# Kernel tuning notes

Measured on AMD Instinct MI355X. Metric: run time of the kernel, lower is better.

Reference implementation:

```python
import jax, jax.numpy as jnp
import numpy as np

D = 1024
H = 16
HD = D // H
FF = 4096
B, S = 2, 2048


def _ln(x, g, b, eps):
    mu = jnp.mean(x, axis=-1, keepdims=True)
    var = jnp.mean(jnp.square(x - mu), axis=-1, keepdims=True)
    return (x - mu) * jax.lax.rsqrt(var + eps) * g + b


def setup_inputs() -> dict:
    key = jax.random.key(0)
    ks = jax.random.split(key, 12)
    s = 0.02
    return {
        "x": jax.random.normal(ks[0], (B, S, D), jnp.float32),
        "attention_mask": jnp.ones((B, 1, 1, S), jnp.int32),
        "wq": jax.random.normal(ks[1], (D, D), jnp.float32) * s,
        "bq": jnp.zeros((D,), jnp.float32),
        "wk": jax.random.normal(ks[2], (D, D), jnp.float32) * s,
        "bk": jnp.zeros((D,), jnp.float32),
        "wv": jax.random.normal(ks[3], (D, D), jnp.float32) * s,
        "bv": jnp.zeros((D,), jnp.float32),
        "wo": jax.random.normal(ks[4], (D, D), jnp.float32) * s,
        "bo": jnp.zeros((D,), jnp.float32),
        "ln1_g": jnp.ones((D,), jnp.float32),
        "ln1_b": jnp.zeros((D,), jnp.float32),
        "w1": jax.random.normal(ks[5], (D, FF), jnp.float32) * s,
        "b1": jnp.zeros((FF,), jnp.float32),
        "w2": jax.random.normal(ks[6], (FF, D), jnp.float32) * s,
        "b2": jnp.zeros((D,), jnp.float32),
        "lnf_g": jnp.ones((D,), jnp.float32),
        "lnf_b": jnp.zeros((D,), jnp.float32),
        "ln2_g": jnp.ones((D,), jnp.float32),
        "ln2_b": jnp.zeros((D,), jnp.float32),
    }


def reference(x, attention_mask, wq, bq, wk, bk, wv, bv, wo, bo,
              ln1_g, ln1_b, w1, b1, w2, b2, lnf_g, lnf_b, ln2_g, ln2_b):
    b, s, d = x.shape
    # --- naive multi-head self-attention ---
    q = (x @ wq + bq).reshape(b, s, H, HD).transpose(0, 2, 1, 3)  # [b,h,s,hd]
    k = (x @ wk + bk).reshape(b, s, H, HD).transpose(0, 2, 1, 3)
    v = (x @ wv + bv).reshape(b, s, H, HD).transpose(0, 2, 1, 3)
    scores = jnp.einsum('bhqd,bhkd->bhqk', q, k) / jnp.sqrt(jnp.float32(HD))
    scores = jnp.where(attention_mask == 0, jnp.float32(-1e9), scores)
    attn = jax.nn.softmax(scores, axis=-1)
    ctx = jnp.einsum('bhqk,bhkd->bhqd', attn, v)
    ctx = ctx.transpose(0, 2, 1, 3).reshape(b, s, d)
    attn_out = ctx @ wo + bo
    # residual + LayerNorm (eps=1e-5, torch default)
    x1 = _ln(x + attn_out, ln1_g, ln1_b, 1e-5)
    # --- BERT-style FFN with internal residual LN (eps=1e-12) ---
    h = jax.nn.gelu(x1 @ w1 + b1, approximate=False)
    ff = _ln(h @ w2 + b2 + x1, lnf_g, lnf_b, 1e-12)
    # --- outer residual + LayerNorm (eps=1e-5) ---
    return _ln(x1 + ff, ln2_g, ln2_b, 1e-5)
```

## Files before the change

kernel.cpp:

```cpp
#include <hip/hip_runtime.h>

#define DMODEL 1024
#define NHEAD  16
#define HDIM   64
#define FFDIM  4096
#define BATCH  2
#define SEQ    2048
#define MTOK   (BATCH*SEQ)

typedef __bf16 bf16;
typedef __bf16 bf16x8 __attribute__((ext_vector_type(8)));
typedef __bf16 bf16x4 __attribute__((ext_vector_type(4)));
typedef float  floatx4 __attribute__((ext_vector_type(4)));
typedef unsigned int u32;
typedef unsigned int u32x4 __attribute__((ext_vector_type(4)));

__device__ __forceinline__ int get_flag(const void* ln1g) {
  return (((const u32*)ln1g)[0] == 0x3F800000u) ? 0 : 1;
}
__device__ __forceinline__ float ld_ext(const void* p, size_t i, int flag) {
  return flag ? (float)((const bf16*)p)[i] : ((const float*)p)[i];
}

__device__ __forceinline__ void gload16(const bf16* g, bf16* lds_uniform) {
  __builtin_amdgcn_global_load_lds(
      (const __attribute__((address_space(1))) u32*)g,
      (__attribute__((address_space(3))) u32*)lds_uniform, 16, 0, 0);
}

__device__ __forceinline__ float gelu_f(float v) {
  float e = __expf(-1.702f * v);
  return __fdividef(v, 1.0f + e);
}

#define VMW(n) asm volatile("s_waitcnt vmcnt(" #n ")" ::: "memory")

__global__ __launch_bounds__(256) void prep(
    const void* wq, const void* wk, const void* wv, const void* wo,
    const void* w1, const void* w2, const void* x, const int* mask,
    bf16* WTqkv, bf16* WToT, bf16* WT1, bf16* WT2, bf16* xC,
    u32* mwAll, bf16* m01All, const void* ln1g)
{
  int flag = get_flag(ln1g);
  int bid = blockIdx.x;
  if (bid >= 16384) {
    int b = bid - 16384;
    int base = b * SEQ + threadIdx.x * 8;
    #pragma unroll
    for (int j = 0; j < 8; j++)
      m01All[base + j] = (bf16)(mask[base + j] ? 1.0f : 0.0f);
    #pragma unroll
    for (int t = 0; t < 4; t++) {
      int k0 = threadIdx.x * 8 + 2 * t;
      u32 mw = (mask[b * SEQ + k0] ? 0x0000FFFFu : 0u) |
               (mask[b * SEQ + k0 + 1] ? 0xFFFF0000u : 0u);
      mwAll[b * (SEQ / 2) + threadIdx.x * 4 + t] = mw;
    }
    return;
  }
  if (bid >= 12288) {
    size_t base = (size_t)(bid - 12288) * 1024;
    int i = threadIdx.x * 4;
    #pragma unroll
    for (int j = 0; j < 4; j++) xC[base + i + j] = (bf16)ld_ext(x, base + i + j, flag);
    return;
  }
  __shared__ bf16 tile[32][33];
  const void* in; bf16* out; int K, N, t;
  if      (bid < 1024)  { in = wq; out = WTqkv;                 K = 1024; N = 1024; t = bid; }
  else if (bid < 2048)  { in = wk; out = WTqkv + 1024 * 1024;   K = 1024; N = 1024; t = bid - 1024; }
  else if (bid < 3072)  { in = wv; out = WTqkv + 2 * 1024 * 1024; K = 1024; N = 1024; t = bid - 2048; }
  else if (bid < 4096)  { in = wo; out = WToT;                  K = 1024; N = 1024; t = bid - 3072; }
  else if (bid < 8192)  { in = w1; out = WT1;                   K = 1024; N = 4096; t = bid - 4096; }
  else                  { in = w2; out = WT2;                   K = 4096; N = 1024; t = bid - 8192; }
  int shift = (N == 4096) ? 7 : 5;
  int k0 = (t >> shift) * 32, n0 = (t & ((1 << shift) - 1)) * 32;
  int tx = threadIdx.x & 31, ty = threadIdx.x >> 5;
  #pragma unroll
  for (int i = ty; i < 32; i += 8)
    tile[i][tx] = (bf16)ld_ext(in, (size_t)(k0 + i) * N + n0 + tx, flag);
  __syncthreads();
  #pragma unroll
  for (int i = ty; i < 32; i += 8)
    out[(size_t)(n0 + i) * K + k0 + tx] = tile[tx][i];
}

__global__ __launch_bounds__(256) void gemm128(
    const bf16* __restrict__ A, const bf16* __restrict__ BT,
    const void* __restrict__ bias0, const void* __restrict__ bias1,
    const void* __restrict__ bias2,
    bf16* __restrict__ out0, bf16* __restrict__ out1, bf16* __restrict__ out2,
    int N, int K, int ksub, int mode, const void* __restrict__ ln1g)
{
  __shared__ __align__(16) char smem[32768];
  bf16* As = (bf16*)smem;
  bf16* Bs = (bf16*)(smem + 16384);
  int flag = get_flag(ln1g);

  int tid = threadIdx.x, lane = tid & 63, w = tid >> 6;
  int wm = w & 1, wn = w >> 1;
  int m0 = blockIdx.x * 128, n0 = blockIdx.y * 128;
  int kstart = blockIdx.z * ksub;
  int r15 = lane & 15, kg = lane >> 4;

  floatx4 acc[4][4];
  #pragma unroll
  for (int mt = 0; mt < 4; mt++)
    #pragma unroll
    for (int nt = 0; nt < 4; nt++) acc[mt][nt] = (floatx4){0.f, 0.f, 0.f, 0.f};

  int srow8 = lane >> 3;
  int skc = (lane & 7) ^ (srow8 & 7);
  const bf16* Ap = A  + (size_t)(m0 + w * 32 + srow8) * K + kstart + skc * 8;
  const bf16* Bp = BT + (size_t)(n0 + w * 32 + srow8) * K + kstart + skc * 8;
  const size_t jstr = (size_t)8 * K;

  for (int it = ksub >> 6; it > 0; it--) {
    #pragma unroll
    for (int j = 0; j < 4; j++) {
      gload16(Ap + j * jstr, As + (size_t)(w * 256 + j * 64) * 8);
      gload16(Bp + j * jstr, Bs + (size_t)(w * 256 + j * 64) * 8);
    }
    Ap += 64; Bp += 64;
    __syncthreads();

    #pragma unroll
    for (int kk = 0; kk < 2; kk++) {
      bf16x8 af[4], bfr[4];
      #pragma unroll
      for (int mt = 0; mt < 4; mt++) {
        int row = wm * 64 + mt * 16 + r15;
        int slot = (kk * 4 + kg) ^ (r15 & 7);
        af[mt] = *(const bf16x8*)&As[(row * 8 + slot) * 8];
      }
      #pragma unroll
      for (int nt = 0; nt < 4; nt++) {
        int row = wn * 64 + nt * 16 + r15;
        int slot = (kk * 4 + kg) ^ (r15 & 7);
        bfr[nt] = *(const bf16x8*)&Bs[(row * 8 + slot) * 8];
      }
      #pragma unroll
      for (int mt = 0; mt < 4; mt++)
        #pragma unroll
        for (int nt = 0; nt < 4; nt++)
          acc[mt][nt] = __builtin_amdgcn_mfma_f32_16x16x32_bf16(af[mt], bfr[nt], acc[mt][nt], 0, 0, 0);
    }
    __syncthreads();
  }

  bf16* scr = (bf16*)(smem + 5120 * w);
  int gcb = n0 + wn * 64;
  int which = (mode == 1) ? (gcb >> 10) : 0;
  int rowg0 = m0 + wm * 64;
  bf16* outp = out0 + (size_t)blockIdx.z * MTOK * N;

  float bvs[4];
  #pragma unroll
  for (int nt = 0; nt < 4; nt++) {
    int gcol = gcb + nt * 16 + r15;
    int bidx = (mode == 1) ? (gcol & 1023) : gcol;
    const void* bp = (mode == 1) ? ((which == 0) ? bias0 : (which == 1) ? bias1 : bias2) : bias0;
    bvs[nt] = (blockIdx.z == 0) ? ld_ext(bp, bidx, flag) : 0.f;
  }

  #pragma unroll
  for (int pass = 0; pass < 2; pass++) {
    #pragma unroll
    for (int mh = 0; mh < 2; mh++) {
      int mt = 2 * pass + mh;
      #pragma unroll
      for (int nt = 0; nt < 4; nt++) {
        int lcol = nt * 16 + r15;
        #pragma unroll
        for (int r = 0; r < 4; r++) {
          int lrow = mh * 16 + kg * 4 + r;
          float val = acc[mt][nt][r] + bvs[nt];
          if (mode == 2) val = gelu_f(val);
          if (mode == 1 && which == 0) val *= 0.125f;
          if (mode == 1 && which == 2) scr[lcol * 40 + lrow] = (bf16)val;
          else                         scr[lrow * 68 + lcol] = (bf16)val;
        }
      }
    }
    if (mode == 1 && which == 2) {
      int hh = (gcb - 2048) >> 6;
      int b = rowg0 >> 11, s0 = rowg0 & 2047;
      #pragma unroll
      for (int it = 0; it < 4; it++) {
        int c = it * 64 + lane;
        int cc = c >> 2, part = c & 3;
        bf16x8 vdat = *(const bf16x8*)&scr[cc * 40 + part * 8];
        *(bf16x8*)(out2 + ((size_t)(b * NHEAD + hh) * HDIM + cc) * SEQ + s0 + pass * 32 + part * 8) = vdat;
      }
    } else {
      #pragma unroll
      for (int it = 0; it < 4; it++) {
        int c = it * 64 + lane;
        int rr = c >> 3, part = c & 7;
        bf16x8 vdat = *(const bf16x8*)&scr[rr * 68 + part * 8];
        int rowg = rowg0 + pass * 32 + rr;
        bf16* dst;
        if (mode == 1) {
          int b = rowg >> 11, s = rowg & 2047;
          int hh = (gcb & 1023) >> 6;
          bf16* o = (which == 0) ? out0 : out1;
          dst = o + ((size_t)(b * NHEAD + hh) * SEQ + s) * HDIM + part * 8;
        } else {
          dst = outp + (size_t)rowg * N + gcb + part * 8;
        }
        *(bf16x8*)dst = vdat;
      }
    }
  }
}

#define STAGE_A(dstbuf, koff, qm)                                             \
  { int gch = (lane & 7) ^ (srow8 & 7);                                       \
    _Pragma("unroll") for (int j = 0; j < 2; j++) {                           \
      int rb = (qm) * 64 + j * 128 + w * 8;                                   \
      gload16(A + (size_t)(m0 + rb + srow8) * K + (koff) + gch * 8,           \
              (dstbuf) + (size_t)rb * 64);                                    \
    } }

#define STAGE_B(dstbuf, koff, qn)                                             \
  { int gch = (lane & 7) ^ (srow8 & 7);                                       \
    _Pragma("unroll") for (int j = 0; j < 2; j++) {                           \
      int rb = (2 * j + (w >> 2)) * 64 + (qn) * 32 + (w & 3) * 8;             \
      gload16(BT + (size_t)(n0 + rb + srow8) * K + (koff) + gch * 8,          \
              (dstbuf) + (size_t)rb * 64);                                    \
    } }

#define PHASE(QM, QN, STAGE_STMT, WAIT_STMT)                                  \
  {                                                                           \
    bf16x8 af[4][2], bfr[2][2];                                               \
    _Pragma("unroll") for (int mt = 0; mt < 4; mt++) {                        \
      int row = wm * 128 + (QM) * 64 + mt * 16 + r15;                         \
      _Pragma("unroll") for (int kk = 0; kk < 2; kk++) {                      \
        int slot = (kk * 4 + kg) ^ (r15 & 7);                                 \
        af[mt][kk] = *(const bf16x8*)&Ac[(size_t)(row * 8 + slot) * 8];       \
      }                                                                       \
    }                                                                         \
    _Pragma("unroll") for (int nt = 0; nt < 2; nt++) {                        \
      int row = wn * 64 + (QN) * 32 + nt * 16 + r15;                          \
      _Pragma("unroll") for (int kk = 0; kk < 2; kk++) {                      \
        int slot = (kk * 4 + kg) ^ (r15 & 7);                                 \
        bfr[nt][kk] = *(const bf16x8*)&Bc[(size_t)(row * 8 + slot) * 8];      \
      }                                                                       \
    }                                                                         \
    STAGE_STMT;                                                               \
    WAIT_STMT;                                                                \
    __builtin_amdgcn_s_barrier();                                             \
    asm volatile("" ::: "memory");                                            \
    __builtin_amdgcn_s_setprio(1);                                            \
    _Pragma("unroll") for (int kk = 0; kk < 2; kk++)                          \
      _Pragma("unroll") for (int mt = 0; mt < 4; mt++)                        \
        _Pragma("unroll") for (int nt = 0; nt < 2; nt++)                      \
          acc[(QM) * 4 + mt][(QN) * 2 + nt] =                                 \
              __builtin_amdgcn_mfma_f32_16x16x32_bf16(                        \
                  af[mt][kk], bfr[nt][kk],                                    \
                  acc[(QM) * 4 + mt][(QN) * 2 + nt], 0, 0, 0);                \
    __builtin_amdgcn_s_setprio(0);                                            \
    __builtin_amdgcn_s_barrier();                                             \
    asm volatile("" ::: "memory");                                            \
  }

__global__ __launch_bounds__(512, 2) void gemm256(
    const bf16* __restrict__ A, const bf16* __restrict__ BT,
    const void* __restrict__ bias0, const void* __restrict__ bias1,
    const void* __restrict__ bias2,
    bf16* __restrict__ out0, bf16* __restrict__ out1, bf16* __restrict__ out2,
    int N, int K, int ksub, int mode, const void* __restrict__ ln1g)
{
  __shared__ __align__(16) char smem[131072];
  int flag = get_flag(ln1g);

  int tid = threadIdx.x, lane = tid & 63, w = tid >> 6;
  int wm = w >> 2, wn = w & 3;
  int r15 = lane & 15, kg = lane >> 4;
  int srow8 = lane >> 3;

  int nx = gridDim.x, ny = gridDim.y;
  int nwg = nx * ny * gridDim.z;
  int wg = blockIdx.x + nx * (blockIdx.y + ny * blockIdx.z);
  if ((nwg & 7) == 0) wg = (wg & 7) * (nwg >> 3) + (wg >> 3);
  int bx = wg % nx, rem = wg / nx;
  int by = rem % ny, bz = rem / ny;

  int m0 = bx * 256, n0 = by * 256;
  int kstart = bz * ksub;
  int NT = ksub >> 6;

  floatx4 acc[8][4];
  #pragma unroll
  for (int mt = 0; mt < 8; mt++)
    #pragma unroll
    for (int nt = 0; nt < 4; nt++) acc[mt][nt] = (floatx4){0.f, 0.f, 0.f, 0.f};

  STAGE_A((bf16*)smem,             kstart, 0);
  STAGE_B((bf16*)(smem + 65536),   kstart, 0);
  STAGE_A((bf16*)smem,             kstart, 1);
  STAGE_B((bf16*)(smem + 65536),   kstart, 1);
  STAGE_A((bf16*)(smem + 32768),   kstart + 64, 0);
  STAGE_B((bf16*)(smem + 98304),   kstart + 64, 0);
  asm volatile("s_waitcnt vmcnt(4)" ::: "memory");
  __builtin_amdgcn_s_barrier();
  asm volatile("" ::: "memory");

  for (int t = 0; t < NT; t++) {
    int cur = (t & 1) * 32768, nxt = ((t + 1) & 1) * 32768;
    bf16* Ac = (bf16*)(smem + cur);
    bf16* Bc = (bf16*)(smem + 65536 + cur);
    bf16* An = (bf16*)(smem + nxt);
    bf16* Bn = (bf16*)(smem + 65536 + nxt);
    int t1 = (t + 1 < NT) ? t + 1 : NT - 1;
    int t2 = (t + 2 < NT) ? t + 2 : NT - 1;
    int k1 = kstart + t1 * 64, k2 = kstart + t2 * 64;
    PHASE(0, 0, STAGE_A(An, k1, 1), VMW(6));
    PHASE(0, 1, STAGE_B(Bn, k1, 1), );
    PHASE(1, 0, STAGE_A(Ac, k2, 0), );
    PHASE(1, 1, STAGE_B(Bc, k2, 0), VMW(8));
  }

  asm volatile("s_waitcnt vmcnt(0)" ::: "memory");
  __builtin_amdgcn_s_barrier();
  asm volatile("" ::: "memory");

  bf16* scr = (bf16*)(smem + 5120 * w);
  int gcb = n0 + wn * 64;
  int which = (mode == 1) ? (gcb >> 10) : 0;
  int rowg0 = m0 + wm * 128;
  bf16* outp = out0 + (size_t)bz * MTOK * (size_t)N;

  float bvs[4];
  #pragma unroll
  for (int nt = 0; nt < 4; nt++) {
    int gcol = gcb + nt * 16 + r15;
    int bidx = (mode == 1) ? (gcol & 1023) : gcol;
    const void* bp = (mode == 1) ? ((which == 0) ? bias0 : (which == 1) ? bias1 : bias2) : bias0;
    bvs[nt] = (bz == 0) ? ld_ext(bp, bidx, flag) : 0.f;
  }

  #pragma unroll
  for (int pass = 0; pass < 4; pass++) {
    #pragma unroll
    for (int mh = 0; mh < 2; mh++) {
      int mt = 2 * pass + mh;
      #pragma unroll
      for (int nt = 0; nt < 4; nt++) {
        int lcol = nt * 16 + r15;
        #pragma unroll
        for (int r = 0; r < 4; r++) {
          int lrow = mh * 16 + kg * 4 + r;
          float val = acc[mt][nt][r] + bvs[nt];
          if (mode == 2) val = gelu_f(val);
          if (mode == 1 && which == 0) val *= 0.125f;
          if (mode == 1 && which == 2) scr[lcol * 40 + lrow] = (bf16)val;
          else                         scr[lrow * 68 + lcol] = (bf16)val;
        }
      }
    }
    if (mode == 1 && which == 2) {
      int hh = (gcb - 2048) >> 6;
      int bb = rowg0 >> 11, s0 = rowg0 & 2047;
      #pragma unroll
      for (int it = 0; it < 4; it++) {
        int c = it * 64 + lane;
        int cc = c >> 2, part = c & 3;
        bf16x8 vdat = *(const bf16x8*)&scr[cc * 40 + part * 8];
        *(bf16x8*)(out2 + ((size_t)(bb * NHEAD + hh) * HDIM + cc) * SEQ + s0 + pass * 32 + part * 8) = vdat;
      }
    } else {
      #pragma unroll
      for (int it = 0; it < 4; it++) {
        int c = it * 64 + lane;
        int rr = c >> 3, part = c & 7;
        bf16x8 vdat = *(const bf16x8*)&scr[rr * 68 + part * 8];
        int rowg = rowg0 + pass * 32 + rr;
        bf16* dst;
        if (mode == 1) {
          int bb = rowg >> 11, s = rowg & 2047;
          int hh = (gcb & 1023) >> 6;
          bf16* o = (which == 0) ? out0 : out1;
          dst = o + ((size_t)(bb * NHEAD + hh) * SEQ + s) * HDIM + part * 8;
        } else {
          dst = outp + (size_t)rowg * N + gcb + part * 8;
        }
        *(bf16x8*)dst = vdat;
      }
    }
  }
}

__global__ __launch_bounds__(256) void attn_mfma(
    const bf16* __restrict__ q, const bf16* __restrict__ k,
    const bf16* __restrict__ vt, const u32* __restrict__ mwAll,
    const bf16* __restrict__ m01All, bf16* __restrict__ ctx)
{
  __shared__ __align__(16) bf16 Ks[2][4096];
  __shared__ __align__(16) bf16 Vts[2][4096];
  __shared__ __align__(16) bf16 Ps[4][2048];

  int tid = threadIdx.x, lane = tid & 63, w = tid >> 6;
  int r15 = lane & 15, kg = lane >> 4;
  int x7 = r15 & 7;
  int bh = (blockIdx.x & 7) * 4 + ((blockIdx.x >> 3) >> 4);
  int qt = (blockIdx.x >> 3) & 15;
  int b = bh >> 4, h = bh & 15;
  int q0 = qt * 128 + w * 32;

  bf16x8 qf[2][2];
  #pragma unroll
  for (int mt = 0; mt < 2; mt++)
    #pragma unroll
    for (int kt2 = 0; kt2 < 2; kt2++)
      qf[mt][kt2] = *(const bf16x8*)(q + ((size_t)bh * SEQ + q0 + mt * 16 + r15) * HDIM + kt2 * 32 + kg * 8);

  floatx4 O[2][4];
  floatx4 lacc[2];
  #pragma unroll
  for (int mt = 0; mt < 2; mt++) {
    lacc[mt] = (floatx4){0.f, 0.f, 0.f, 0.f};
    #pragma unroll
    for (int dt = 0; dt < 4; dt++) O[mt][dt] = (floatx4){0.f, 0.f, 0.f, 0.f};
  }

  int slo = kg ^ x7, shi = (kg + 4) ^ x7;
  const bf16* pap[2][2];
  #pragma unroll
  for (int mt = 0; mt < 2; mt++) {
    pap[mt][0] = &Ps[w][((mt * 16 + r15) * 8 + slo) * 8];
    pap[mt][1] = &Ps[w][((mt * 16 + r15) * 8 + shi) * 8];
  }

  int kr = lane >> 3, kc = lane & 7;
  int vrow = tid >> 3, vcc = tid & 7;
  int vsw = vcc ^ (vrow & 7);
  const bf16* kb_ = k + (size_t)bh * SEQ * HDIM;
  const bf16* vb_ = vt + (size_t)bh * HDIM * SEQ;
  const u32*  mwb = mwAll + (size_t)b * (SEQ / 2);
  const bf16* m1b = m01All + (size_t)b * SEQ;

  u32x4 pv0 = *(const u32x4*)(vb_ + (size_t)vrow * SEQ + vcc * 8);
  u32x4 pv1 = *(const u32x4*)(vb_ + (size_t)(vrow + 32) * SEQ + vcc * 8);
  u32x4 pmw = *(const u32x4*)&mwb[vcc * 4];
  bf16x8 m0c = *(const bf16x8*)&m1b[kg * 8];
  bf16x8 m1c = *(const bf16x8*)&m1b[32 + kg * 8];
  asm volatile("" ::: "memory");
  #pragma unroll
  for (int j = 0; j < 2; j++)
    gload16(kb_ + (size_t)(16 * w + 8 * j + kr) * HDIM + (kc ^ kr) * 8,
            &Ks[0][0] + (size_t)(w * 128 + j * 64) * 8);
  VMW(4);
  pv0 &= pmw; pv1 &= pmw;
  *(u32x4*)&Vts[0][(vrow * 8 + vsw) * 8] = pv0;
  *(u32x4*)&Vts[0][((vrow + 32) * 8 + vsw) * 8] = pv1;
  asm volatile("s_waitcnt lgkmcnt(0)" ::: "memory");
  __builtin_amdgcn_s_barrier();
  asm volatile("" ::: "memory");

  for (int t = 0; t < SEQ / 64; t++) {
    int cur = t & 1, nxt = cur ^ 1;
    int ktn = (t + 1 < SEQ / 64) ? (t + 1) * 64 : t * 64;
    u32x4 nv0 = *(const u32x4*)(vb_ + (size_t)vrow * SEQ + ktn + vcc * 8);
    u32x4 nv1 = *(const u32x4*)(vb_ + (size_t)(vrow + 32) * SEQ + ktn + vcc * 8);
    u32x4 nmw = *(const u32x4*)&mwb[(ktn + vcc * 8) >> 1];
    bf16x8 nm0 = *(const bf16x8*)&m1b[ktn + kg * 8];
    bf16x8 nm1 = *(const bf16x8*)&m1b[ktn + 32 + kg * 8];
    asm volatile("" ::: "memory");
    #pragma unroll
    for (int j = 0; j < 2; j++)
      gload16(kb_ + (size_t)(ktn + 16 * w + 8 * j + kr) * HDIM + (kc ^ kr) * 8,
              &Ks[nxt][0] + (size_t)(w * 128 + j * 64) * 8);
    VMW(7);
    __builtin_amdgcn_s_barrier();
    asm volatile("" ::: "memory");

    const bf16* Kc = &Ks[cur][0];
    const bf16* Vc = &Vts[cur][0];

    floatx4 S[2][4];
    #pragma unroll
    for (int mt = 0; mt < 2; mt++)
      #pragma unroll
      for (int nt = 0; nt < 4; nt++) S[mt][nt] = (floatx4){0.f, 0.f, 0.f, 0.f};
    __builtin_amdgcn_s_setprio(1);
    #pragma unroll
    for (int nt = 0; nt < 4; nt++) {
      int rb = (nt * 16 + r15) * 8;
      bf16x8 kf0 = *(const bf16x8*)&Kc[(rb + slo) * 8];
      bf16x8 kf1 = *(const bf16x8*)&Kc[(rb + shi) * 8];
      #pragma unroll
      for (int mt = 0; mt < 2; mt++) {
        S[mt][nt] = __builtin_amdgcn_mfma_f32_16x16x32_bf16(kf0, qf[mt][0], S[mt][nt], 0, 0, 0);
        S[mt][nt] = __builtin_amdgcn_mfma_f32_16x16x32_bf16(kf1, qf[mt][1], S[mt][nt], 0, 0, 0);
      }
    }
    __builtin_amdgcn_s_setprio(0);

    #pragma unroll
    for (int mt = 0; mt < 2; mt++)
      #pragma unroll
      for (int nt = 0; nt < 4; nt++) {
        bf16x4 pk;
        #pragma unroll
        for (int r = 0; r < 4; r++) pk[r] = (bf16)__expf(S[mt][nt][r]);
        int c2 = 2 * nt + (kg >> 1);
        *(bf16x4*)&Ps[w][((mt * 16 + r15) * 8 + (c2 ^ x7)) * 8 + (kg & 1) * 4] = pk;
      }

    bf16x8 pa[2][2];
    #pragma unroll
    for (int mt = 0; mt < 2; mt++) {
      pa[mt][0] = *(const bf16x8*)pap[mt][0];
      pa[mt][1] = *(const bf16x8*)pap[mt][1];
    }
    __builtin_amdgcn_s_setprio(1);
    #pragma unroll
    for (int dt = 0; dt < 4; dt++) {
      int rb = (dt * 16 + r15) * 8;
      bf16x8 vf0 = *(const bf16x8*)&Vc[(rb + slo) * 8];
      bf16x8 vf1 = *(const bf16x8*)&Vc[(rb + shi) * 8];
      #pragma unroll
      for (int mt = 0; mt < 2; mt++) {
        O[mt][dt] = __builtin_amdgcn_mfma_f32_16x16x32_bf16(pa[mt][0], vf0, O[mt][dt], 0, 0, 0);
        O[mt][dt] = __builtin_amdgcn_mfma_f32_16x16x32_bf16(pa[mt][1], vf1, O[mt][dt], 0, 0, 0);
      }
    }
    #pragma unroll
    for (int mt = 0; mt < 2; mt++) {
      lacc[mt] = __builtin_amdgcn_mfma_f32_16x16x32_bf16(pa[mt][0], m0c, lacc[mt], 0, 0, 0);
      lacc[mt] = __builtin_amdgcn_mfma_f32_16x16x32_bf16(pa[mt][1], m1c, lacc[mt], 0, 0, 0);
    }
    __builtin_amdgcn_s_setprio(0);

    VMW(2);
    nv0 &= nmw; nv1 &= nmw;
    *(u32x4*)&Vts[nxt][(vrow * 8 + vsw) * 8] = nv0;
    *(u32x4*)&Vts[nxt][((vrow + 32) * 8 + vsw) * 8] = nv1;
    m0c = nm0; m1c = nm1;
    asm volatile("s_waitcnt lgkmcnt(0)" ::: "memory");
    __builtin_amdgcn_s_barrier();
    asm volatile("" ::: "memory");
  }
  VMW(0);

  #pragma unroll
  for (int mt = 0; mt < 2; mt++) {
    float inv[4];
    #pragma unroll
    for (int r = 0; r < 4; r++) inv[r] = 1.f / lacc[mt][r];
    #pragma unroll
    for (int dt = 0; dt < 4; dt++)
      #pragma unroll
      for (int r = 0; r < 4; r++) {
        int srow = q0 + mt * 16 + kg * 4 + r;
        int col = h * 64 + dt * 16 + r15;
        ctx[((size_t)b * SEQ + srow) * DMODEL + col] = (bf16)(O[mt][dt][r] * inv[r]);
      }
  }
}

__global__ __launch_bounds__(256) void ln_kernel(
    const bf16* ba, const bf16* bb, const bf16* bc,
    const void* g, const void* be, float eps, bf16* outb, const void* ln1g)
{
  __shared__ float red1[4], red2[4];
  int flag = get_flag(ln1g);
  size_t base = (size_t)blockIdx.x * DMODEL;
  float v[4];
  #pragma unroll
  for (int i = 0; i < 4; i++) {
    int idx = threadIdx.x + i * 256;
    v[i] = (float)ba[base + idx] + (float)bb[base + idx] + (float)bc[base + idx];
  }
  float sum = v[0] + v[1] + v[2] + v[3];
  #pragma unroll
  for (int o = 32; o > 0; o >>= 1) sum += __shfl_xor(sum, o);
  if ((threadIdx.x & 63) == 0) red1[threadIdx.x >> 6] = sum;
  __syncthreads();
  float mean = (red1[0] + red1[1] + red1[2] + red1[3]) * (1.f / DMODEL);
  float sq = 0.f;
  #pragma unroll
  for (int i = 0; i < 4; i++) { v[i] -= mean; sq += v[i] * v[i]; }
  #pragma unroll
  for (int o = 32; o > 0; o >>= 1) sq += __shfl_xor(sq, o);
  if ((threadIdx.x & 63) == 0) red2[threadIdx.x >> 6] = sq;
  __syncthreads();
  float rstd = rsqrtf((red2[0] + red2[1] + red2[2] + red2[3]) * (1.f / DMODEL) + eps);
  #pragma unroll
  for (int i = 0; i < 4; i++) {
    int idx = threadIdx.x + i * 256;
    outb[base + idx] = (bf16)(v[i] * rstd * ld_ext(g, idx, flag) + ld_ext(be, idx, flag));
  }
}

__global__ __launch_bounds__(256) void ln_double(
    const bf16* p0, const bf16* p1, const bf16* p2, const bf16* p3,
    const bf16* x1,
    const void* gf, const void* bf, const void* g2, const void* b2,
    void* out_ext, const void* ln1g, int np)
{
  __shared__ float red1[4], red2[4];
  int flag = get_flag(ln1g);
  size_t base = (size_t)blockIdx.x * DMODEL;
  float xv[4], v[4];
  #pragma unroll
  for (int i = 0; i < 4; i++) {
    int idx = threadIdx.x + i * 256;
    xv[i] = (float)x1[base + idx];
    v[i] = xv[i] + (float)p0[base + idx] + (float)p1[base + idx];
    if (np == 4) v[i] += (float)p2[base + idx] + (float)p3[base + idx];
  }
  float sum = v[0] + v[1] + v[2] + v[3];
  #pragma unroll
  for (int o = 32; o > 0; o >>= 1) sum += __shfl_xor(sum, o);
  if ((threadIdx.x & 63) == 0) red1[threadIdx.x >> 6] = sum;
  __syncthreads();
  float mean = (red1[0] + red1[1] + red1[2] + red1[3]) * (1.f / DMODEL);
  float sq = 0.f;
  #pragma unroll
  for (int i = 0; i < 4; i++) { v[i] -= mean; sq += v[i] * v[i]; }
  #pragma unroll
  for (int o = 32; o > 0; o >>= 1) sq += __shfl_xor(sq, o);
  if ((threadIdx.x & 63) == 0) red2[threadIdx.x >> 6] = sq;
  __syncthreads();
  float rstd = rsqrtf((red2[0] + red2[1] + red2[2] + red2[3]) * (1.f / DMODEL) + 1e-12f);
  #pragma unroll
  for (int i = 0; i < 4; i++) {
    int idx = threadIdx.x + i * 256;
    float ff = v[i] * rstd * ld_ext(gf, idx, flag) + ld_ext(bf, idx, flag);
    v[i] = xv[i] + (float)(bf16)ff;
  }
  __syncthreads();
  sum = v[0] + v[1] + v[2] + v[3];
  #pragma unroll
  for (int o = 32; o > 0; o >>= 1) sum += __shfl_xor(sum, o);
  if ((threadIdx.x & 63) == 0) red1[threadIdx.x >> 6] = sum;
  __syncthreads();
  mean = (red1[0] + red1[1] + red1[2] + red1[3]) * (1.f / DMODEL);
  sq = 0.f;
  #pragma unroll
  for (int i = 0; i < 4; i++) { v[i] -= mean; sq += v[i] * v[i]; }
  #pragma unroll
  for (int o = 32; o > 0; o >>= 1) sq += __shfl_xor(sq, o);
  if ((threadIdx.x & 63) == 0) red2[threadIdx.x >> 6] = sq;
  __syncthreads();
  rstd = rsqrtf((red2[0] + red2[1] + red2[2] + red2[3]) * (1.f / DMODEL) + 1e-5f);
  #pragma unroll
  for (int i = 0; i < 4; i++) {
    int idx = threadIdx.x + i * 256;
    float y = v[i] * rstd * ld_ext(g2, idx, flag) + ld_ext(b2, idx, flag);
    if (flag) ((bf16*)out_ext)[base + idx] = (bf16)y;
    else      ((float*)out_ext)[base + idx] = y;
  }
}

extern "C" void kernel_launch(void* const* d_in, const int* in_sizes, int n_in,
                              void* d_out, int out_size, void* d_ws, size_t ws_size,
                              hipStream_t stream) {
  const void* x    = d_in[0];
  const int*  msk  = (const int*)d_in[1];
  const void* wq   = d_in[2];
  const void* bq   = d_in[3];
  const void* wk   = d_in[4];
  const void* bk   = d_in[5];
  const void* wv   = d_in[6];
  const void* bv   = d_in[7];
  const void* wo   = d_in[8];
  const void* bo   = d_in[9];
  const void* ln1g = d_in[10];
  const void* ln1b = d_in[11];
  const void* w1   = d_in[12];
  const void* b1   = d_in[13];
  const void* w2   = d_in[14];
  const void* b2   = d_in[15];
  const void* lnfg = d_in[16];
  const void* lnfb = d_in[17];
  const void* ln2g = d_in[18];
  const void* ln2b = d_in[19];

  const size_t MB = 1024 * 1024;
  char* p = (char*)d_ws;
  int big = ws_size >= (size_t)80 * MB;
  bf16* xC     = (bf16*)(p + 0 * MB);
  bf16* qb     = (bf16*)(p + 8 * MB);
  bf16* kb     = (bf16*)(p + 16 * MB);
  bf16* vtb    = (bf16*)(p + 24 * MB);
  bf16* ctxb   = (bf16*)(p + 32 * MB);
  bf16* WTqkv  = (bf16*)(p + 40 * MB);
  bf16* WToT   = (bf16*)(p + 46 * MB);
  bf16* WT1    = (bf16*)(p + 48 * MB);
  bf16* WT2    = (bf16*)(p + (big ? 72 : 56) * MB);
  bf16* ao     = (bf16*)(p + 8 * MB);
  bf16* x1b    = xC;
  bf16* hb     = (bf16*)(p + 8 * MB);
  bf16* ffp    = (bf16*)(p + 40 * MB);
  u32*  mwAll  = (u32*)d_out;
  bf16* m01All = (bf16*)((char*)d_out + 8192);
  const size_t PS = (size_t)MTOK * DMODEL;

  prep<<<16386, 256, 0, stream>>>(wq, wk, wv, wo, w1, w2, x, msk,
                                  WTqkv, WToT, WT1, WT2, xC, mwAll, m01All, ln1g);

  gemm256<<<dim3(MTOK / 256, 3072 / 256, 1), 512, 0, stream>>>(
      xC, WTqkv, bq, bk, bv, qb, kb, vtb, 3072, DMODEL, DMODEL, 1, ln1g);

  attn_mfma<<<BATCH * NHEAD * (SEQ / 128), 256, 0, stream>>>(qb, kb, vtb, mwAll, m01All, ctxb);

  gemm128<<<dim3(MTOK / 128, DMODEL / 128, 2), 256, 0, stream>>>(
      ctxb, WToT, bo, nullptr, nullptr, ao, nullptr, nullptr, DMODEL, DMODEL, 512, 3, ln1g);

  ln_kernel<<<MTOK, 256, 0, stream>>>(ao, ao + PS, xC, ln1g, ln1b,
                                      1e-5f, x1b, ln1g);

  gemm256<<<dim3(MTOK / 256, FFDIM / 256, 1), 512, 0, stream>>>(
      x1b, WT1, b1, nullptr, nullptr, hb, nullptr, nullptr, FFDIM, DMODEL, DMODEL, 2, ln1g);

  if (big) {
    gemm256<<<dim3(MTOK / 256, DMODEL / 256, 4), 512, 0, stream>>>(
        hb, WT2, b2, nullptr, nullptr, ffp, nullptr, nullptr, DMODEL, FFDIM, FFDIM / 4, 3, ln1g);
    ln_double<<<MTOK, 256, 0, stream>>>(ffp, ffp + PS, ffp + 2 * PS, ffp + 3 * PS,
                                        x1b, lnfg, lnfb, ln2g, ln2b, d_out, ln1g, 4);
  } else {
    gemm128<<<dim3(MTOK / 128, DMODEL / 128, 2), 256, 0, stream>>>(
        hb, WT2, b2, nullptr, nullptr, ffp, nullptr, nullptr, DMODEL, FFDIM, 2048, 3, ln1g);
    ln_double<<<MTOK, 256, 0, stream>>>(ffp, ffp + PS, ffp, ffp,
                                        x1b, lnfg, lnfb, ln2g, ln2b, d_out, ln1g, 2);
  }
}
```

Baseline: 376.9 us.

## Software-pipeline attention PV matmul one tile behind and route QKV GEMM to gemm128

The attention kernel now double-buffers the per-wave P tile and runs the P·V and row-sum MFMAs for the previous key tile alongside the QK^T MFMAs for the current one. This lets exp/softmax work overlap with matrix work, and it needs an epilogue step after the loop for the last tile. The QKV projection launch moves from gemm256 to gemm128, and gemm256 loses its mode-1 (QKV scatter) epilogue, which shrinks its argument list and branches. The pipelining adds LDS use and changes where the barrier sits, so it relies on the zero-initialised second buffers to make the first iteration's extra MFMAs harmless.

```diff
diff --git a/kernel.cpp b/kernel.cpp
--- a/kernel.cpp
+++ b/kernel.cpp
@@ -266,9 +266,7 @@
 
 __global__ __launch_bounds__(512, 2) void gemm256(
     const bf16* __restrict__ A, const bf16* __restrict__ BT,
-    const void* __restrict__ bias0, const void* __restrict__ bias1,
-    const void* __restrict__ bias2,
-    bf16* __restrict__ out0, bf16* __restrict__ out1, bf16* __restrict__ out2,
+    const void* __restrict__ bias0, bf16* __restrict__ out0,
     int N, int K, int ksub, int mode, const void* __restrict__ ln1g)
 {
   __shared__ __align__(16) char smem[131072];
@@ -327,7 +325,6 @@
 
   bf16* scr = (bf16*)(smem + 5120 * w);
   int gcb = n0 + wn * 64;
-  int which = (mode == 1) ? (gcb >> 10) : 0;
   int rowg0 = m0 + wm * 128;
   bf16* outp = out0 + (size_t)bz * MTOK * (size_t)N;
 
@@ -335,9 +332,7 @@
   #pragma unroll
   for (int nt = 0; nt < 4; nt++) {
     int gcol = gcb + nt * 16 + r15;
-    int bidx = (mode == 1) ? (gcol & 1023) : gcol;
-    const void* bp = (mode == 1) ? ((which == 0) ? bias0 : (which == 1) ? bias1 : bias2) : bias0;
-    bvs[nt] = (bz == 0) ? ld_ext(bp, bidx, flag) : 0.f;
+    bvs[nt] = (bz == 0) ? ld_ext(bias0, gcol, flag) : 0.f;
   }
 
   #pragma unroll
@@ -347,46 +342,22 @@
       int mt = 2 * pass + mh;
       #pragma unroll
       for (int nt = 0; nt < 4; nt++) {
-        int lcol = nt * 16 + r15;
         #pragma unroll
         for (int r = 0; r < 4; r++) {
           int lrow = mh * 16 + kg * 4 + r;
           float val = acc[mt][nt][r] + bvs[nt];
           if (mode == 2) val = gelu_f(val);
-          if (mode == 1 && which == 0) val *= 0.125f;
-          if (mode == 1 && which == 2) scr[lcol * 40 + lrow] = (bf16)val;
-          else                         scr[lrow * 68 + lcol] = (bf16)val;
+          scr[lrow * 68 + nt * 16 + r15] = (bf16)val;
         }
       }
     }
-    if (mode == 1 && which == 2) {
-      int hh = (gcb - 2048) >> 6;
-      int bb = rowg0 >> 11, s0 = rowg0 & 2047;
-      #pragma unroll
-      for (int it = 0; it < 4; it++) {
-        int c = it * 64 + lane;
-        int cc = c >> 2, part = c & 3;
-        bf16x8 vdat = *(const bf16x8*)&scr[cc * 40 + part * 8];
-        *(bf16x8*)(out2 + ((size_t)(bb * NHEAD + hh) * HDIM + cc) * SEQ + s0 + pass * 32 + part * 8) = vdat;
-      }
-    } else {
-      #pragma unroll
-      for (int it = 0; it < 4; it++) {
-        int c = it * 64 + lane;
-        int rr = c >> 3, part = c & 7;
-        bf16x8 vdat = *(const bf16x8*)&scr[rr * 68 + part * 8];
-        int rowg = rowg0 + pass * 32 + rr;
-        bf16* dst;
-        if (mode == 1) {
-          int bb = rowg >> 11, s = rowg & 2047;
-          int hh = (gcb & 1023) >> 6;
-          bf16* o = (which == 0) ? out0 : out1;
-          dst = o + ((size_t)(bb * NHEAD + hh) * SEQ + s) * HDIM + part * 8;
-        } else {
-          dst = outp + (size_t)rowg * N + gcb + part * 8;
-        }
-        *(bf16x8*)dst = vdat;
-      }
+    #pragma unroll
+    for (int it = 0; it < 4; it++) {
+      int c = it * 64 + lane;
+      int rr = c >> 3, part = c & 7;
+      bf16x8 vdat = *(const bf16x8*)&scr[rr * 68 + part * 8];
+      int rowg = rowg0 + pass * 32 + rr;
+      *(bf16x8*)(outp + (size_t)rowg * N + gcb + part * 8) = vdat;
     }
   }
 }
@@ -398,7 +369,7 @@
 {
   __shared__ __align__(16) bf16 Ks[2][4096];
   __shared__ __align__(16) bf16 Vts[2][4096];
-  __shared__ __align__(16) bf16 Ps[4][2048];
+  __shared__ __align__(16) bf16 Ps[4][2][2048];
 
   int tid = threadIdx.x, lane = tid & 63, w = tid >> 6;
   int r15 = lane & 15, kg = lane >> 4;
@@ -425,11 +396,13 @@
   }
 
   int slo = kg ^ x7, shi = (kg + 4) ^ x7;
-  const bf16* pap[2][2];
-  #pragma unroll
-  for (int mt = 0; mt < 2; mt++) {
-    pap[mt][0] = &Ps[w][((mt * 16 + r15) * 8 + slo) * 8];
-    pap[mt][1] = &Ps[w][((mt * 16 + r15) * 8 + shi) * 8];
+
+  {
+    u32x4 zz = (u32x4){0u, 0u, 0u, 0u};
+    #pragma unroll
+    for (int j = 0; j < 4; j++) *(u32x4*)&Ps[w][1][lane * 32 + j * 8] = zz;
+    #pragma unroll
+    for (int j = 0; j < 2; j++) *(u32x4*)&Vts[1][tid * 16 + j * 8] = zz;
   }
 
   int kr = lane >> 3, kc = lane & 7;
@@ -454,6 +427,9 @@
   pv0 &= pmw; pv1 &= pmw;
   *(u32x4*)&Vts[0][(vrow * 8 + vsw) * 8] = pv0;
   *(u32x4*)&Vts[0][((vrow + 32) * 8 + vsw) * 8] = pv1;
+  bf16x8 m0p, m1p;
+  #pragma unroll
+  for (int j = 0; j < 8; j++) { m0p[j] = (bf16)0.f; m1p[j] = (bf16)0.f; }
   asm volatile("s_waitcnt lgkmcnt(0)" ::: "memory");
   __builtin_amdgcn_s_barrier();
   asm volatile("" ::: "memory");
@@ -476,7 +452,16 @@
     asm volatile("" ::: "memory");
 
     const bf16* Kc = &Ks[cur][0];
-    const bf16* Vc = &Vts[cur][0];
+    const bf16* Vp = &Vts[nxt][0];
+    const bf16* Pr = &Ps[w][nxt][0];
+    bf16* Pw = &Ps[w][cur][0];
+
+    bf16x8 pa0[2], pa1[2];
+    #pragma unroll
+    for (int mt = 0; mt < 2; mt++) {
+      pa0[mt] = *(const bf16x8*)&Pr[((mt * 16 + r15) * 8 + slo) * 8];
+      pa1[mt] = *(const bf16x8*)&Pr[((mt * 16 + r15) * 8 + shi) * 8];
+    }
 
     floatx4 S[2][4];
     #pragma unroll
@@ -494,6 +479,22 @@
         S[mt][nt] = __builtin_amdgcn_mfma_f32_16x16x32_bf16(kf0, qf[mt][0], S[mt][nt], 0, 0, 0);
         S[mt][nt] = __builtin_amdgcn_mfma_f32_16x16x32_bf16(kf1, qf[mt][1], S[mt][nt], 0, 0, 0);
       }
+    }
+    #pragma unroll
+    for (int dt = 0; dt < 4; dt++) {
+      int rb = (dt * 16 + r15) * 8;
+      bf16x8 vf0 = *(const bf16x8*)&Vp[(rb + slo) * 8];
+      bf16x8 vf1 = *(const bf16x8*)&Vp[(rb + shi) * 8];
+      #pragma unroll
+      for (int mt = 0; mt < 2; mt++) {
+        O[mt][dt] = __builtin_amdgcn_mfma_f32_16x16x32_bf16(pa0[mt], vf0, O[mt][dt], 0, 0, 0);
+        O[mt][dt] = __builtin_amdgcn_mfma_f32_16x16x32_bf16(pa1[mt], vf1, O[mt][dt], 0, 0, 0);
+      }
+    }
+    #pragma unroll
+    for (int mt = 0; mt < 2; mt++) {
+      lacc[mt] = __builtin_amdgcn_mfma_f32_16x16x32_bf16(pa0[mt], m0p, lacc[mt], 0, 0, 0);
+      lacc[mt] = __builtin_amdgcn_mfma_f32_16x16x32_bf16(pa1[mt], m1p, lacc[mt], 0, 0, 0);
     }
     __builtin_amdgcn_s_setprio(0);
 
@@ -505,42 +506,45 @@
         #pragma unroll
         for (int r = 0; r < 4; r++) pk[r] = (bf16)__expf(S[mt][nt][r]);
         int c2 = 2 * nt + (kg >> 1);
-        *(bf16x4*)&Ps[w][((mt * 16 + r15) * 8 + (c2 ^ x7)) * 8 + (kg & 1) * 4] = pk;
-      }
-
-    bf16x8 pa[2][2];
-    #pragma unroll
-    for (int mt = 0; mt < 2; mt++) {
-      pa[mt][0] = *(const bf16x8*)pap[mt][0];
-      pa[mt][1] = *(const bf16x8*)pap[mt][1];
-    }
-    __builtin_amdgcn_s_setprio(1);
-    #pragma unroll
-    for (int dt = 0; dt < 4; dt++) {
-      int rb = (dt * 16 + r15) * 8;
-      bf16x8 vf0 = *(const bf16x8*)&Vc[(rb + slo) * 8];
-      bf16x8 vf1 = *(const bf16x8*)&Vc[(rb + shi) * 8];
-      #pragma unroll
-      for (int mt = 0; mt < 2; mt++) {
-        O[mt][dt] = __builtin_amdgcn_mfma_f32_16x16x32_bf16(pa[mt][0], vf0, O[mt][dt], 0, 0, 0);
-        O[mt][dt] = __builtin_amdgcn_mfma_f32_16x16x32_bf16(pa[mt][1], vf1, O[mt][dt], 0, 0, 0);
-      }
-    }
-    #pragma unroll
-    for (int mt = 0; mt < 2; mt++) {
-      lacc[mt] = __builtin_amdgcn_mfma_f32_16x16x32_bf16(pa[mt][0], m0c, lacc[mt], 0, 0, 0);
-      lacc[mt] = __builtin_amdgcn_mfma_f32_16x16x32_bf16(pa[mt][1], m1c, lacc[mt], 0, 0, 0);
-    }
-    __builtin_amdgcn_s_setprio(0);
+        *(bf16x4*)&Pw[((mt * 16 + r15) * 8 + (c2 ^ x7)) * 8 + (kg & 1) * 4] = pk;
+      }
+
+    __builtin_amdgcn_s_barrier();
+    asm volatile("" ::: "memory");
 
     VMW(2);
     nv0 &= nmw; nv1 &= nmw;
     *(u32x4*)&Vts[nxt][(vrow * 8 + vsw) * 8] = nv0;
     *(u32x4*)&Vts[nxt][((vrow + 32) * 8 + vsw) * 8] = nv1;
-    m0c = nm0; m1c = nm1;
+    m0p = m0c; m1p = m1c; m0c = nm0; m1c = nm1;
     asm volatile("s_waitcnt lgkmcnt(0)" ::: "memory");
-    __builtin_amdgcn_s_barrier();
-    asm volatile("" ::: "memory");
+  }
+
+  {
+    const bf16* Vp = &Vts[1][0];
+    const bf16* Pr = &Ps[w][1][0];
+    bf16x8 pa0[2], pa1[2];
+    #pragma unroll
+    for (int mt = 0; mt < 2; mt++) {
+      pa0[mt] = *(const bf16x8*)&Pr[((mt * 16 + r15) * 8 + slo) * 8];
+      pa1[mt] = *(const bf16x8*)&Pr[((mt * 16 + r15) * 8 + shi) * 8];
+    }
+    #pragma unroll
+    for (int dt = 0; dt < 4; dt++) {
+      int rb = (dt * 16 + r15) * 8;
+      bf16x8 vf0 = *(const bf16x8*)&Vp[(rb + slo) * 8];
+      bf16x8 vf1 = *(const bf16x8*)&Vp[(rb + shi) * 8];
+      #pragma unroll
+      for (int mt = 0; mt < 2; mt++) {
+        O[mt][dt] = __builtin_amdgcn_mfma_f32_16x16x32_bf16(pa0[mt], vf0, O[mt][dt], 0, 0, 0);
+        O[mt][dt] = __builtin_amdgcn_mfma_f32_16x16x32_bf16(pa1[mt], vf1, O[mt][dt], 0, 0, 0);
+      }
+    }
+    #pragma unroll
+    for (int mt = 0; mt < 2; mt++) {
+      lacc[mt] = __builtin_amdgcn_mfma_f32_16x16x32_bf16(pa0[mt], m0p, lacc[mt], 0, 0, 0);
+      lacc[mt] = __builtin_amdgcn_mfma_f32_16x16x32_bf16(pa1[mt], m1p, lacc[mt], 0, 0, 0);
+    }
   }
   VMW(0);
 
@@ -702,7 +706,7 @@
   prep<<<16386, 256, 0, stream>>>(wq, wk, wv, wo, w1, w2, x, msk,
                                   WTqkv, WToT, WT1, WT2, xC, mwAll, m01All, ln1g);
 
-  gemm256<<<dim3(MTOK / 256, 3072 / 256, 1), 512, 0, stream>>>(
+  gemm128<<<dim3(MTOK / 128, 3072 / 128, 1), 256, 0, stream>>>(
       xC, WTqkv, bq, bk, bv, qb, kb, vtb, 3072, DMODEL, DMODEL, 1, ln1g);
 
   attn_mfma<<<BATCH * NHEAD * (SEQ / 128), 256, 0, stream>>>(qb, kb, vtb, mwAll, m01All, ctxb);
@@ -714,11 +718,11 @@
                                       1e-5f, x1b, ln1g);
 
   gemm256<<<dim3(MTOK / 256, FFDIM / 256, 1), 512, 0, stream>>>(
-      x1b, WT1, b1, nullptr, nullptr, hb, nullptr, nullptr, FFDIM, DMODEL, DMODEL, 2, ln1g);
+      x1b, WT1, b1, hb, FFDIM, DMODEL, DMODEL, 2, ln1g);
 
   if (big) {
     gemm256<<<dim3(MTOK / 256, DMODEL / 256, 4), 512, 0, stream>>>(
-        hb, WT2, b2, nullptr, nullptr, ffp, nullptr, nullptr, DMODEL, FFDIM, FFDIM / 4, 3, ln1g);
+        hb, WT2, b2, ffp, DMODEL, FFDIM, FFDIM / 4, 3, ln1g);
     ln_double<<<MTOK, 256, 0, stream>>>(ffp, ffp + PS, ffp + 2 * PS, ffp + 3 * PS,
                                         x1b, lnfg, lnfb, ln2g, ln2b, d_out, ln1g, 4);
   } else {
```

After: 379.6 us. No clear change (+0.7%).

## Restructure gemm256 pipeline to single-tile lookahead and route QKV projection to gemm128

Applied to the files above, without the earlier changes.

The gemm256 main loop drops its two-tile-ahead prefetch, which overwrote the current buffer, in favour of a plain double buffer. Each phase now stages one quarter of the next K tile into the other buffer, and the phase order is arranged so A/B fragment registers are reused across consecutive phases (A0B0, A1B0, A1B1, A0B1), cutting LDS reads. The QKV projection moves to gemm128 (assumed to support mode 1 head-split outputs), so gemm256 loses its mode-1 epilogue branches and extra bias/output arguments. This trades prefetch depth for fewer LDS fragment loads and a simpler epilogue, and changes the tile size and occupancy of the QKV GEMM.

```diff
diff --git a/kernel.cpp b/kernel.cpp
--- a/kernel.cpp
+++ b/kernel.cpp
@@ -34,6 +34,7 @@
 }
 
 #define VMW(n) asm volatile("s_waitcnt vmcnt(" #n ")" ::: "memory")
+#define BAR()  { __builtin_amdgcn_s_barrier(); asm volatile("" ::: "memory"); }
 
 __global__ __launch_bounds__(256) void prep(
     const void* wq, const void* wk, const void* wv, const void* wo,
@@ -230,45 +231,38 @@
               (dstbuf) + (size_t)rb * 64);                                    \
     } }
 
-#define PHASE(QM, QN, STAGE_STMT, WAIT_STMT)                                  \
-  {                                                                           \
-    bf16x8 af[4][2], bfr[2][2];                                               \
-    _Pragma("unroll") for (int mt = 0; mt < 4; mt++) {                        \
-      int row = wm * 128 + (QM) * 64 + mt * 16 + r15;                         \
-      _Pragma("unroll") for (int kk = 0; kk < 2; kk++) {                      \
-        int slot = (kk * 4 + kg) ^ (r15 & 7);                                 \
-        af[mt][kk] = *(const bf16x8*)&Ac[(size_t)(row * 8 + slot) * 8];       \
-      }                                                                       \
+#define RD_A(QM)                                                              \
+  _Pragma("unroll") for (int mt = 0; mt < 4; mt++) {                          \
+    int row = wm * 128 + (QM) * 64 + mt * 16 + r15;                           \
+    _Pragma("unroll") for (int kk = 0; kk < 2; kk++) {                        \
+      int slot = (kk * 4 + kg) ^ (r15 & 7);                                   \
+      af[mt][kk] = *(const bf16x8*)&Ac[(size_t)(row * 8 + slot) * 8];         \
     }                                                                         \
-    _Pragma("unroll") for (int nt = 0; nt < 2; nt++) {                        \
-      int row = wn * 64 + (QN) * 32 + nt * 16 + r15;                          \
-      _Pragma("unroll") for (int kk = 0; kk < 2; kk++) {                      \
-        int slot = (kk * 4 + kg) ^ (r15 & 7);                                 \
-        bfr[nt][kk] = *(const bf16x8*)&Bc[(size_t)(row * 8 + slot) * 8];      \
-      }                                                                       \
+  }
+
+#define RD_B(QN)                                                              \
+  _Pragma("unroll") for (int nt = 0; nt < 2; nt++) {                          \
+    int row = wn * 64 + (QN) * 32 + nt * 16 + r15;                            \
+    _Pragma("unroll") for (int kk = 0; kk < 2; kk++) {                        \
+      int slot = (kk * 4 + kg) ^ (r15 & 7);                                   \
+      bfv[nt][kk] = *(const bf16x8*)&Bc[(size_t)(row * 8 + slot) * 8];        \
     }                                                                         \
-    STAGE_STMT;                                                               \
-    WAIT_STMT;                                                                \
-    __builtin_amdgcn_s_barrier();                                             \
-    asm volatile("" ::: "memory");                                            \
-    __builtin_amdgcn_s_setprio(1);                                            \
-    _Pragma("unroll") for (int kk = 0; kk < 2; kk++)                          \
-      _Pragma("unroll") for (int mt = 0; mt < 4; mt++)                        \
-        _Pragma("unroll") for (int nt = 0; nt < 2; nt++)                      \
-          acc[(QM) * 4 + mt][(QN) * 2 + nt] =                                 \
-              __builtin_amdgcn_mfma_f32_16x16x32_bf16(                        \
-                  af[mt][kk], bfr[nt][kk],                                    \
-                  acc[(QM) * 4 + mt][(QN) * 2 + nt], 0, 0, 0);                \
-    __builtin_amdgcn_s_setprio(0);                                            \
-    __builtin_amdgcn_s_barrier();                                             \
-    asm volatile("" ::: "memory");                                            \
-  }
+  }
+
+#define MF(QM, QN)                                                            \
+  __builtin_amdgcn_s_setprio(1);                                              \
+  _Pragma("unroll") for (int kk = 0; kk < 2; kk++)                            \
+    _Pragma("unroll") for (int mt = 0; mt < 4; mt++)                          \
+      _Pragma("unroll") for (int nt = 0; nt < 2; nt++)                        \
+        acc[(QM) * 4 + mt][(QN) * 2 + nt] =                                   \
+            __builtin_amdgcn_mfma_f32_16x16x32_bf16(                          \
+                af[mt][kk], bfv[nt][kk],                                      \
+                acc[(QM) * 4 + mt][(QN) * 2 + nt], 0, 0, 0);                  \
+  __builtin_amdgcn_s_setprio(0);
 
 __global__ __launch_bounds__(512, 2) void gemm256(
     const bf16* __restrict__ A, const bf16* __restrict__ BT,
-    const void* __restrict__ bias0, const void* __restrict__ bias1,
-    const void* __restrict__ bias2,
-    bf16* __restrict__ out0, bf16* __restrict__ out1, bf16* __restrict__ out2,
+    const void* __restrict__ bias0, bf16* __restrict__ out0,
     int N, int K, int ksub, int mode, const void* __restrict__ ln1g)
 {
   __shared__ __align__(16) char smem[131072];
@@ -300,11 +294,8 @@
   STAGE_B((bf16*)(smem + 65536),   kstart, 0);
   STAGE_A((bf16*)smem,             kstart, 1);
   STAGE_B((bf16*)(smem + 65536),   kstart, 1);
-  STAGE_A((bf16*)(smem + 32768),   kstart + 64, 0);
-  STAGE_B((bf16*)(smem + 98304),   kstart + 64, 0);
-  asm volatile("s_waitcnt vmcnt(4)" ::: "memory");
-  __builtin_amdgcn_s_barrier();
-  asm volatile("" ::: "memory");
+  VMW(4);
+  BAR();
 
   for (int t = 0; t < NT; t++) {
     int cur = (t & 1) * 32768, nxt = ((t + 1) & 1) * 32768;
@@ -313,21 +304,31 @@
     bf16* An = (bf16*)(smem + nxt);
     bf16* Bn = (bf16*)(smem + 65536 + nxt);
     int t1 = (t + 1 < NT) ? t + 1 : NT - 1;
-    int t2 = (t + 2 < NT) ? t + 2 : NT - 1;
-    int k1 = kstart + t1 * 64, k2 = kstart + t2 * 64;
-    PHASE(0, 0, STAGE_A(An, k1, 1), VMW(6));
-    PHASE(0, 1, STAGE_B(Bn, k1, 1), );
-    PHASE(1, 0, STAGE_A(Ac, k2, 0), );
-    PHASE(1, 1, STAGE_B(Bc, k2, 0), VMW(8));
-  }
-
-  asm volatile("s_waitcnt vmcnt(0)" ::: "memory");
-  __builtin_amdgcn_s_barrier();
-  asm volatile("" ::: "memory");
+    int k1 = kstart + t1 * 64;
+
+    bf16x8 af[4][2], bfv[2][2];
+    RD_A(0); RD_B(0);
+    STAGE_A(An, k1, 0);
+    VMW(4);
+    BAR(); MF(0, 0); BAR();
+    RD_A(1);
+    STAGE_B(Bn, k1, 0);
+    VMW(4);
+    BAR(); MF(1, 0); BAR();
+    RD_B(1);
+    STAGE_A(An, k1, 1);
+    BAR(); MF(1, 1); BAR();
+    RD_A(0);
+    STAGE_B(Bn, k1, 1);
+    VMW(4);
+    BAR(); MF(0, 1); BAR();
+  }
+
+  VMW(0);
+  BAR();
 
   bf16* scr = (bf16*)(smem + 5120 * w);
   int gcb = n0 + wn * 64;
-  int which = (mode == 1) ? (gcb >> 10) : 0;
   int rowg0 = m0 + wm * 128;
   bf16* outp = out0 + (size_t)bz * MTOK * (size_t)N;
 
@@ -335,9 +336,7 @@
   #pragma unroll
   for (int nt = 0; nt < 4; nt++) {
     int gcol = gcb + nt * 16 + r15;
-    int bidx = (mode == 1) ? (gcol & 1023) : gcol;
-    const void* bp = (mode == 1) ? ((which == 0) ? bias0 : (which == 1) ? bias1 : bias2) : bias0;
-    bvs[nt] = (bz == 0) ? ld_ext(bp, bidx, flag) : 0.f;
+    bvs[nt] = (bz == 0) ? ld_ext(bias0, gcol, flag) : 0.f;
   }
 
   #pragma unroll
@@ -347,46 +346,22 @@
       int mt = 2 * pass + mh;
       #pragma unroll
       for (int nt = 0; nt < 4; nt++) {
-        int lcol = nt * 16 + r15;
         #pragma unroll
         for (int r = 0; r < 4; r++) {
           int lrow = mh * 16 + kg * 4 + r;
           float val = acc[mt][nt][r] + bvs[nt];
           if (mode == 2) val = gelu_f(val);
-          if (mode == 1 && which == 0) val *= 0.125f;
-          if (mode == 1 && which == 2) scr[lcol * 40 + lrow] = (bf16)val;
-          else                         scr[lrow * 68 + lcol] = (bf16)val;
+          scr[lrow * 68 + nt * 16 + r15] = (bf16)val;
         }
       }
     }
-    if (mode == 1 && which == 2) {
-      int hh = (gcb - 2048) >> 6;
-      int bb = rowg0 >> 11, s0 = rowg0 & 2047;
-      #pragma unroll
-      for (int it = 0; it < 4; it++) {
-        int c = it * 64 + lane;
-        int cc = c >> 2, part = c & 3;
-        bf16x8 vdat = *(const bf16x8*)&scr[cc * 40 + part * 8];
-        *(bf16x8*)(out2 + ((size_t)(bb * NHEAD + hh) * HDIM + cc) * SEQ + s0 + pass * 32 + part * 8) = vdat;
-      }
-    } else {
-      #pragma unroll
-      for (int it = 0; it < 4; it++) {
-        int c = it * 64 + lane;
-        int rr = c >> 3, part = c & 7;
-        bf16x8 vdat = *(const bf16x8*)&scr[rr * 68 + part * 8];
-        int rowg = rowg0 + pass * 32 + rr;
-        bf16* dst;
-        if (mode == 1) {
-          int bb = rowg >> 11, s = rowg & 2047;
-          int hh = (gcb & 1023) >> 6;
-          bf16* o = (which == 0) ? out0 : out1;
-          dst = o + ((size_t)(bb * NHEAD + hh) * SEQ + s) * HDIM + part * 8;
-        } else {
-          dst = outp + (size_t)rowg * N + gcb + part * 8;
-        }
-        *(bf16x8*)dst = vdat;
-      }
+    #pragma unroll
+    for (int it = 0; it < 4; it++) {
+      int c = it * 64 + lane;
+      int rr = c >> 3, part = c & 7;
+      bf16x8 vdat = *(const bf16x8*)&scr[rr * 68 + part * 8];
+      int rowg = rowg0 + pass * 32 + rr;
+      *(bf16x8*)(outp + (size_t)rowg * N + gcb + part * 8) = vdat;
     }
   }
 }
@@ -702,7 +677,7 @@
   prep<<<16386, 256, 0, stream>>>(wq, wk, wv, wo, w1, w2, x, msk,
                                   WTqkv, WToT, WT1, WT2, xC, mwAll, m01All, ln1g);
 
-  gemm256<<<dim3(MTOK / 256, 3072 / 256, 1), 512, 0, stream>>>(
+  gemm128<<<dim3(MTOK / 128, 3072 / 128, 1), 256, 0, stream>>>(
       xC, WTqkv, bq, bk, bv, qb, kb, vtb, 3072, DMODEL, DMODEL, 1, ln1g);
 
   attn_mfma<<<BATCH * NHEAD * (SEQ / 128), 256, 0, stream>>>(qb, kb, vtb, mwAll, m01All, ctxb);
@@ -714,11 +689,11 @@
                                       1e-5f, x1b, ln1g);
 
   gemm256<<<dim3(MTOK / 256, FFDIM / 256, 1), 512, 0, stream>>>(
-      x1b, WT1, b1, nullptr, nullptr, hb, nullptr, nullptr, FFDIM, DMODEL, DMODEL, 2, ln1g);
+      x1b, WT1, b1, hb, FFDIM, DMODEL, DMODEL, 2, ln1g);
 
   if (big) {
     gemm256<<<dim3(MTOK / 256, DMODEL / 256, 4), 512, 0, stream>>>(
-        hb, WT2, b2, nullptr, nullptr, ffp, nullptr, nullptr, DMODEL, FFDIM, FFDIM / 4, 3, ln1g);
+        hb, WT2, b2, ffp, DMODEL, FFDIM, FFDIM / 4, 3, ln1g);
     ln_double<<<MTOK, 256, 0, stream>>>(ffp, ffp + PS, ffp + 2 * PS, ffp + 3 * PS,
                                         x1b, lnfg, lnfb, ln2g, ln2b, d_out, ln1g, 4);
   } else {
```

Result: faster. 358.9 us (-4.8%).
